# Optimization experiments

Hardware: AMD Instinct MI355X
Metric: run time of the kernel (lower is better)

## Reference

```python
import math
import jax, jax.numpy as jnp
import numpy as np

B, L, D, H = 2, 2048, 1024, 16
HD = D // H
EPS = 1e-6
ROPE_BASE = 10000.0


def setup_inputs() -> dict:
    key = jax.random.key(0)
    ks = jax.random.split(key, 6)
    s = 0.02
    return {
        "z_H_previous": jax.random.normal(ks[0], (B, L, D), jnp.float32),
        "z_L_current": jax.random.normal(ks[1], (B, L, D), jnp.float32),
        "w_qkv": jax.random.normal(ks[2], (3 * D, D), jnp.float32) * s,
        "w_out": jax.random.normal(ks[3], (D, D), jnp.float32) * s,
        "w_ffn1": jax.random.normal(ks[4], (4 * D, D), jnp.float32) * s,
        "w_ffn2": jax.random.normal(ks[5], (D, 4 * D), jnp.float32) * s,
        "g_norm1": jnp.ones((D,), jnp.float32),
        "g_norm2": jnp.ones((D,), jnp.float32),
    }


def _rmsnorm(x, g):
    # mean of squares over last dim, rsqrt, scale
    ms = jnp.mean(x * x, axis=-1, keepdims=True)
    return x * jax.lax.rsqrt(ms + EPS) * g


def _rope(x):
    # x: [b, h, l, hd]; non-interleaved rotate-half RoPE
    l, d = x.shape[-2], x.shape[-1]
    half = d // 2
    inv_freq = 1.0 / (ROPE_BASE ** (jnp.arange(half, dtype=jnp.float32) / half))
    freqs = jnp.arange(l, dtype=jnp.float32)[:, None] * inv_freq[None, :]  # [l, half]
    cos, sin = jnp.cos(freqs), jnp.sin(freqs)
    x1, x2 = x[..., :half], x[..., half:]
    return jnp.concatenate([x1 * cos - x2 * sin, x2 * cos + x1 * sin], axis=-1)


def reference(z_H_previous, z_L_current, w_qkv, w_out, w_ffn1, w_ffn2, g_norm1, g_norm2):
    x = z_H_previous + z_L_current                       # [b, l, d]
    h = _rmsnorm(x, g_norm1)
    b, l, d = h.shape
    qkv = h @ w_qkv.T                                    # [b, l, 3d]
    qkv = qkv.reshape(b, l, 3, H, HD).transpose(2, 0, 3, 1, 4)  # [3, b, h, l, hd]
    q, k, v = qkv[0], qkv[1], qkv[2]
    q = _rope(q)
    k = _rope(k)
    scores = jnp.einsum("bhqd,bhkd->bhqk", q, k) / math.sqrt(HD)
    attn = jax.nn.softmax(scores, axis=-1)
    out = jnp.einsum("bhqk,bhkd->bhqd", attn, v)         # [b, h, l, hd]
    out = out.transpose(0, 2, 1, 3).reshape(b, l, d)
    x = x + out @ w_out.T
    h2 = _rmsnorm(x, g_norm2)
    ffn = jax.nn.silu(h2 @ w_ffn1.T) @ w_ffn2.T
    return x + ffn
```

## Files before the change

### kernel.cpp

```cpp
#include <hip/hip_runtime.h>

typedef __bf16 bf16;
typedef __bf16 bf16x2 __attribute__((ext_vector_type(2)));
typedef __bf16 bf16x8 __attribute__((ext_vector_type(8)));
typedef __bf16 bf16x4 __attribute__((ext_vector_type(4)));
typedef float  f32x4  __attribute__((ext_vector_type(4)));
typedef float  f32x16 __attribute__((ext_vector_type(16)));
typedef unsigned int uint;

static __device__ __forceinline__ void async_copy16(const void* g, void* l) {
  __builtin_amdgcn_global_load_lds((__attribute__((address_space(1))) void*)g,
                                   (__attribute__((address_space(3))) void*)l,
                                   16, 0, 0);
}

static __device__ __forceinline__ uint pkbf2(float a, float b) {
  union { bf16x2 v; uint u; } x;
  x.v[0] = (bf16)a; x.v[1] = (bf16)b;
  return x.u;
}

union U4 { uint u[4]; bf16x8 v; };

__global__ __launch_bounds__(256)
void f2b_all(const float* __restrict__ s0, const float* __restrict__ s1,
             const float* __restrict__ s2, const float* __restrict__ s3,
             bf16* __restrict__ d0, bf16* __restrict__ d1,
             bf16* __restrict__ d2, bf16* __restrict__ d3) {
  int i = blockIdx.x * 256 + threadIdx.x;
  const float* s; bf16* d; int j;
  if (i < 786432)       { s = s0; d = d0; j = i; }
  else if (i < 1048576) { s = s1; d = d1; j = i - 786432; }
  else if (i < 2097152) { s = s2; d = d2; j = i - 1048576; }
  else                  { s = s3; d = d3; j = i - 2097152; }
  float4 v = ((const float4*)s)[j];
  bf16x4 o;
  o[0] = (bf16)v.x; o[1] = (bf16)v.y; o[2] = (bf16)v.z; o[3] = (bf16)v.w;
  ((bf16x4*)d)[j] = o;
}

__global__ __launch_bounds__(256)
void add_rmsnorm_kernel(const float* __restrict__ a, const float* __restrict__ b,
                        const float* __restrict__ g, float* __restrict__ xout,
                        bf16* __restrict__ hout) {
  const int row = blockIdx.x;
  const int tid = threadIdx.x;
  const size_t base = (size_t)row * 1024 + tid * 4;
  float4 x = *(const float4*)(a + base);
  if (b) {
    float4 y = *(const float4*)(b + base);
    x.x += y.x; x.y += y.y; x.z += y.z; x.w += y.w;
  }
  float ss = x.x*x.x + x.y*x.y + x.z*x.z + x.w*x.w;
#pragma unroll
  for (int off = 32; off > 0; off >>= 1) ss += __shfl_xor(ss, off, 64);
  __shared__ float red[4];
  const int wave = tid >> 6, lane = tid & 63;
  if (lane == 0) red[wave] = ss;
  __syncthreads();
  const float total = red[0] + red[1] + red[2] + red[3];
  const float scale = rsqrtf(total * (1.0f / 1024.0f) + 1e-6f);
  if (xout) *(float4*)(xout + base) = x;
  float4 gv = *(const float4*)(g + tid * 4);
  bf16x4 h;
  h[0] = (bf16)(x.x * scale * gv.x);
  h[1] = (bf16)(x.y * scale * gv.y);
  h[2] = (bf16)(x.z * scale * gv.z);
  h[3] = (bf16)(x.w * scale * gv.w);
  *(bf16x4*)(hout + base) = h;
}

enum { EP_QKV = 0, EP_ADD_RESID = 1, EP_SILU = 2 };

template <int MODE>
__global__ __launch_bounds__(256)
void gemm_bt(const bf16* __restrict__ A, const bf16* __restrict__ W,
             const float* __restrict__ resid, float* __restrict__ outF,
             bf16* __restrict__ outB, bf16* __restrict__ outB2,
             int M, int N, int K) {
  __shared__ bf16 As[128 * 64];
  __shared__ bf16 Bs[128 * 64];
  const int tid  = threadIdx.x;
  const int wave = tid >> 6;
  const int lane = tid & 63;
  const int quad = lane >> 4;
  const int l16  = lane & 15;

  const int bm = blockIdx.x & 31;
  const int bn = blockIdx.x >> 5;
  const int m0 = bm << 7, n0 = bn << 7;
  const int wm = (wave >> 1) << 6;
  const int wn = (wave & 1) << 6;

  const int rl = lane >> 3;
  const int cg = (lane & 7) ^ rl;
  const bf16* gA = A + (size_t)(m0 + wave * 32 + rl) * K + cg * 8;
  const bf16* gB = W + (size_t)(n0 + wave * 32 + rl) * K + cg * 8;

  const int s8 = l16 & 7;
  f32x4 acc[4][4] = {};

  for (int k0 = 0; k0 < K; k0 += 64) {
    __syncthreads();
#pragma unroll
    for (int i = 0; i < 4; i++) {
      async_copy16(gA + (size_t)(i * 8) * K, &As[(wave * 32 + i * 8) * 64]);
      async_copy16(gB + (size_t)(i * 8) * K, &Bs[(wave * 32 + i * 8) * 64]);
    }
    gA += 64; gB += 64;
    __syncthreads();
#pragma unroll
    for (int kh = 0; kh < 2; kh++) {
      bf16x8 af[4], bfr[4];
#pragma unroll
      for (int i = 0; i < 4; i++)
        af[i] = *(const bf16x8*)&As[(wm + i * 16 + l16) * 64 + (((kh * 4 + quad) ^ s8) * 8)];
#pragma unroll
      for (int j = 0; j < 4; j++)
        bfr[j] = *(const bf16x8*)&Bs[(wn + j * 16 + l16) * 64 + (((kh * 4 + quad) ^ s8) * 8)];
#pragma unroll
      for (int i = 0; i < 4; i++)
#pragma unroll
        for (int j = 0; j < 4; j++)
          acc[i][j] = __builtin_amdgcn_mfma_f32_16x16x32_bf16(af[i], bfr[j], acc[i][j], 0, 0, 0);
    }
  }

  if constexpr (MODE == EP_QKV) {
    const int which = n0 >> 10;
    if (which == 2) {
#pragma unroll
      for (int i = 0; i < 4; i++) {
        const int mbase = m0 + wm + i * 16 + quad * 4;
#pragma unroll
        for (int j = 0; j < 4; j++) {
          const int n = n0 + wn + j * 16 + l16;
          const int hh = (n >> 6) & 15, hd = n & 63;
#pragma unroll
          for (int r = 0; r < 4; r++) {
            const int m = mbase + r;
            const int bb = m >> 11, l = m & 2047;
            outB2[((size_t)(bb * 16 + hh) * 64 + hd) * 2048 + l] = (bf16)acc[i][j][r];
          }
        }
      }
    } else {
      const float sc = (which == 0) ? 0.1803368801111243f : 1.0f;
#pragma unroll
      for (int jp = 0; jp < 2; jp++) {
        const int hd1 = jp * 16 + l16;
        const float invf = exp2f(-0.4152410118609203f * (float)hd1);
        const int n1 = n0 + wn + jp * 16 + l16;
        const int hh = (n1 >> 6) & 15;
#pragma unroll
        for (int i = 0; i < 4; i++) {
          const int mbase = m0 + wm + i * 16 + quad * 4;
#pragma unroll
          for (int r = 0; r < 4; r++) {
            const int m = mbase + r;
            const int bb = m >> 11, l = m & 2047;
            float sv, cv;
            sincosf((float)l * invf, &sv, &cv);
            const float x1 = acc[i][jp][r], x2 = acc[i][jp + 2][r];
            const size_t base = (((size_t)(which * 2 + bb) * 16 + hh) * 2048 + l) * 64;
            outB[base + hd1]      = (bf16)((x1 * cv - x2 * sv) * sc);
            outB[base + hd1 + 32] = (bf16)((x2 * cv + x1 * sv) * sc);
          }
        }
      }
    }
  } else {
#pragma unroll
    for (int i = 0; i < 4; i++) {
      const int mbase = m0 + wm + i * 16 + quad * 4;
#pragma unroll
      for (int j = 0; j < 4; j++) {
        const int n = n0 + wn + j * 16 + l16;
        f32x4 v = acc[i][j];
#pragma unroll
        for (int r = 0; r < 4; r++) {
          const int m = mbase + r;
          const float val = v[r];
          if constexpr (MODE == EP_ADD_RESID) {
            outF[(size_t)m * N + n] = val + resid[(size_t)m * N + n];
          } else {
            outB[(size_t)m * N + n] = (bf16)(val / (1.0f + __expf(-val)));
          }
        }
      }
    }
  }
}

__global__ __launch_bounds__(256)
void gemm_bt_splitk(const bf16* __restrict__ A, const bf16* __restrict__ W,
                    float* __restrict__ P, int M, int N, int Ktot) {
  __shared__ bf16 As[128 * 64];
  __shared__ bf16 Bs[128 * 64];
  const int tid  = threadIdx.x;
  const int wave = tid >> 6;
  const int lane = tid & 63;
  const int quad = lane >> 4;
  const int l16  = lane & 15;

  const int r6 = blockIdx.x & 63;
  const int bn = blockIdx.x >> 6;
  const int bm = r6 >> 1;
  const int split = r6 & 1;
  const int m0 = bm << 7, n0 = bn << 7;
  const int wm = (wave >> 1) << 6;
  const int wn = (wave & 1) << 6;
  const int Kh = Ktot >> 1;
  const int koff = split * Kh;

  const int rl = lane >> 3;
  const int cg = (lane & 7) ^ rl;
  const bf16* gA = A + (size_t)(m0 + wave * 32 + rl) * Ktot + koff + cg * 8;
  const bf16* gB = W + (size_t)(n0 + wave * 32 + rl) * Ktot + koff + cg * 8;

  const int s8 = l16 & 7;
  f32x4 acc[4][4] = {};

  for (int k0 = 0; k0 < Kh; k0 += 64) {
    __syncthreads();
#pragma unroll
    for (int i = 0; i < 4; i++) {
      async_copy16(gA + (size_t)(i * 8) * Ktot, &As[(wave * 32 + i * 8) * 64]);
      async_copy16(gB + (size_t)(i * 8) * Ktot, &Bs[(wave * 32 + i * 8) * 64]);
    }
    gA += 64; gB += 64;
    __syncthreads();
#pragma unroll
    for (int kh = 0; kh < 2; kh++) {
      bf16x8 af[4], bfr[4];
#pragma unroll
      for (int i = 0; i < 4; i++)
        af[i] = *(const bf16x8*)&As[(wm + i * 16 + l16) * 64 + (((kh * 4 + quad) ^ s8) * 8)];
#pragma unroll
      for (int j = 0; j < 4; j++)
        bfr[j] = *(const bf16x8*)&Bs[(wn + j * 16 + l16) * 64 + (((kh * 4 + quad) ^ s8) * 8)];
#pragma unroll
      for (int i = 0; i < 4; i++)
#pragma unroll
        for (int j = 0; j < 4; j++)
          acc[i][j] = __builtin_amdgcn_mfma_f32_16x16x32_bf16(af[i], bfr[j], acc[i][j], 0, 0, 0);
    }
  }

  float* Pd = P + (size_t)split * M * N;
#pragma unroll
  for (int i = 0; i < 4; i++) {
    const int mbase = m0 + wm + i * 16 + quad * 4;
#pragma unroll
    for (int j = 0; j < 4; j++) {
      const int n = n0 + wn + j * 16 + l16;
#pragma unroll
      for (int r = 0; r < 4; r++)
        Pd[(size_t)(mbase + r) * N + n] = acc[i][j][r];
    }
  }
}

__global__ __launch_bounds__(256)
void splitk_combine(const float* __restrict__ P, const float* __restrict__ resid,
                    float* __restrict__ out, int total4) {
  int i = blockIdx.x * 256 + threadIdx.x;
  if (i < total4) {
    float4 a = ((const float4*)P)[i];
    float4 b = ((const float4*)(P + 4194304))[i];
    float4 r = ((const float4*)resid)[i];
    float4 o;
    o.x = a.x + b.x + r.x; o.y = a.y + b.y + r.y;
    o.z = a.z + b.z + r.z; o.w = a.w + b.w + r.w;
    ((float4*)out)[i] = o;
  }
}

__global__ __launch_bounds__(256)
void gemm64_bt(const bf16* __restrict__ A, const bf16* __restrict__ W,
               const float* __restrict__ resid, float* __restrict__ outF,
               int M, int N, int K) {
  __shared__ bf16 As[64 * 64];
  __shared__ bf16 Bs[128 * 64];
  const int tid = threadIdx.x, wave = tid >> 6, lane = tid & 63;
  const int quad = lane >> 4, l16 = lane & 15;
  const int bm = blockIdx.x & 63;
  const int bn = blockIdx.x >> 6;
  const int m0 = bm << 6, n0 = bn << 7;
  const int wm = (wave >> 1) * 32, wn = (wave & 1) * 64;

  const int rl = lane >> 3;
  const int cg = (lane & 7) ^ rl;
  const bf16* gA = A + (size_t)(m0 + wave * 16 + rl) * K + cg * 8;
  const bf16* gB = W + (size_t)(n0 + wave * 32 + rl) * K + cg * 8;

  const int s8 = l16 & 7;
  f32x4 acc[2][4] = {};
  for (int k0 = 0; k0 < K; k0 += 64) {
    __syncthreads();
#pragma unroll
    for (int i = 0; i < 2; i++)
      async_copy16(gA + (size_t)(i * 8) * K, &As[(wave * 16 + i * 8) * 64]);
#pragma unroll
    for (int i = 0; i < 4; i++)
      async_copy16(gB + (size_t)(i * 8) * K, &Bs[(wave * 32 + i * 8) * 64]);
    gA += 64; gB += 64;
    __syncthreads();
#pragma unroll
    for (int kh = 0; kh < 2; kh++) {
      bf16x8 af[2], bfr[4];
#pragma unroll
      for (int i = 0; i < 2; i++)
        af[i] = *(const bf16x8*)&As[(wm + i * 16 + l16) * 64 + (((kh * 4 + quad) ^ s8) * 8)];
#pragma unroll
      for (int j = 0; j < 4; j++)
        bfr[j] = *(const bf16x8*)&Bs[(wn + j * 16 + l16) * 64 + (((kh * 4 + quad) ^ s8) * 8)];
#pragma unroll
      for (int i = 0; i < 2; i++)
#pragma unroll
        for (int j = 0; j < 4; j++)
          acc[i][j] = __builtin_amdgcn_mfma_f32_16x16x32_bf16(af[i], bfr[j], acc[i][j], 0, 0, 0);
    }
  }
#pragma unroll
  for (int i = 0; i < 2; i++) {
    const int mbase = m0 + wm + i * 16 + quad * 4;
#pragma unroll
    for (int j = 0; j < 4; j++) {
      const int n = n0 + wn + j * 16 + l16;
#pragma unroll
      for (int r = 0; r < 4; r++) {
        const int m = mbase + r;
        outF[(size_t)m * N + n] = acc[i][j][r] + resid[(size_t)m * N + n];
      }
    }
  }
}

__global__ __launch_bounds__(256, 4)
void attn_kernel(const bf16* __restrict__ qk, const bf16* __restrict__ vt,
                 bf16* __restrict__ Opart, float* __restrict__ Lpart) {
  const int qt    = blockIdx.x & 15;
  const int bh    = (blockIdx.x >> 4) & 31;
  const int split = blockIdx.x >> 9;
  const bf16* Qp = qk + (size_t)bh * 131072;
  const bf16* Kp = Qp + 4194304;
  const bf16* Vp = vt + (size_t)bh * 131072;

  const int tid = threadIdx.x, wave = tid >> 6, lane = tid & 63;
  const int hl = lane >> 5, l32 = lane & 31;
  const int qw = qt * 128 + wave * 32;

  __shared__ bf16 lds[8192];
  bf16* Ks = lds;
  bf16* Vs = lds + 4096;

  bf16x8 qf[4];
#pragma unroll
  for (int dk = 0; dk < 4; dk++)
    qf[dk] = *(const bf16x8*)&Qp[(size_t)(qw + l32) * 64 + dk * 16 + hl * 8];

  f32x16 o0 = {}, o1 = {};
  float sum_acc = 0.0f;

  const int rl = lane >> 3;
  const int cg = (lane & 7) ^ rl;

  const int kvbase = split * 512;
  for (int kv0 = kvbase; kv0 < kvbase + 512; kv0 += 64) {
    __syncthreads();
#pragma unroll
    for (int i = 0; i < 2; i++) {
      const int row = wave * 16 + i * 8;
      async_copy16(Kp + (size_t)(kv0 + row + rl) * 64 + cg * 8, &Ks[row * 64]);
      async_copy16(Vp + (size_t)(row + rl) * 2048 + kv0 + cg * 8, &Vs[row * 64]);
    }
    __syncthreads();

    U4 pf[4];
#pragma unroll
    for (int ks = 0; ks < 2; ks++) {
      f32x16 s = {};
#pragma unroll
      for (int dk = 0; dk < 4; dk++) {
        const bf16x8 kf = *(const bf16x8*)
            &Ks[(ks * 32 + l32) * 64 + ((dk * 2 + hl) ^ (l32 & 7)) * 8];
        s = __builtin_amdgcn_mfma_f32_32x32x16_bf16(kf, qf[dk], s, 0, 0, 0);
      }
      uint d[8];
#pragma unroll
      for (int i = 0; i < 8; i++) {
        const float a = exp2f(s[2 * i]);
        const float b = exp2f(s[2 * i + 1]);
        sum_acc += a + b;
        d[i] = pkbf2(a, b);
      }
      uint send0 = hl ? d[0] : d[2];
      uint send1 = hl ? d[1] : d[3];
      uint send2 = hl ? d[4] : d[6];
      uint send3 = hl ? d[5] : d[7];
      const uint r0 = __shfl_xor(send0, 32, 64);
      const uint r1 = __shfl_xor(send1, 32, 64);
      const uint r2 = __shfl_xor(send2, 32, 64);
      const uint r3 = __shfl_xor(send3, 32, 64);
      U4& f0 = pf[ks * 2];
      U4& f1 = pf[ks * 2 + 1];
      f0.u[0] = hl ? r0 : d[0];  f0.u[1] = hl ? r1 : d[1];
      f0.u[2] = hl ? d[2] : r0;  f0.u[3] = hl ? d[3] : r1;
      f1.u[0] = hl ? r2 : d[4];  f1.u[1] = hl ? r3 : d[5];
      f1.u[2] = hl ? d[6] : r2;  f1.u[3] = hl ? d[7] : r3;
    }

#pragma unroll
    for (int c16 = 0; c16 < 4; c16++) {
      const bf16x8 vf0 = *(const bf16x8*)&Vs[l32 * 64 + ((c16 * 2 + hl) ^ (l32 & 7)) * 8];
      const bf16x8 vf1 = *(const bf16x8*)&Vs[(32 + l32) * 64 + ((c16 * 2 + hl) ^ (l32 & 7)) * 8];
      o0 = __builtin_amdgcn_mfma_f32_32x32x16_bf16(vf0, pf[c16].v, o0, 0, 0, 0);
      o1 = __builtin_amdgcn_mfma_f32_32x32x16_bf16(vf1, pf[c16].v, o1, 0, 0, 0);
    }
  }

  const float l_i = sum_acc + __shfl_xor(sum_acc, 32, 64);
  Lpart[(size_t)(split * 32 + bh) * 2048 + qt * 128 + wave * 32 + l32] = l_i;

  uint* L32 = (uint*)lds;
#pragma unroll
  for (int p = 0; p < 2; p++) {
    __syncthreads();
    if ((wave >> 1) == p) {
      const int lrow = (wave & 1) * 32 + l32;
#pragma unroll
      for (int ds = 0; ds < 2; ds++) {
        const f32x16 ov = ds ? o1 : o0;
#pragma unroll
        for (int i = 0; i < 8; i++) {
          const int r = 2 * i;
          const int dd = ds * 32 + (r & 3) + 8 * (r >> 2) + 4 * hl;
          L32[lrow * 36 + (dd >> 1)] = pkbf2(ov[r], ov[r + 1]);
        }
      }
    }
    __syncthreads();
#pragma unroll
    for (int sp = 0; sp < 2; sp++) {
      const int qr = sp * 32 + (tid >> 3), c = tid & 7;
      const uint4 v = *(const uint4*)&L32[qr * 36 + c * 4];
      *(uint4*)&Opart[(((size_t)(split * 32 + bh) * 2048) + qt * 128 + p * 64 + qr) * 64 + c * 8] = v;
    }
  }
}

__global__ __launch_bounds__(256)
void attn_combine(const bf16* __restrict__ Opart, const float* __restrict__ Lpart,
                  bf16* __restrict__ out) {
  const int t = blockIdx.x * 256 + threadIdx.x;
  const int c = t & 7, qq = t >> 3;
  const int bh = qq >> 11, q = qq & 2047;
  const int b = bh >> 4, h = bh & 15;
  float acc[8] = {};
  float lsum = 0.0f;
#pragma unroll
  for (int s = 0; s < 4; s++) {
    const bf16x8 ov = *(const bf16x8*)&Opart[((size_t)(s * 32 + bh) * 2048 + q) * 64 + c * 8];
    lsum += Lpart[(size_t)(s * 32 + bh) * 2048 + q];
#pragma unroll
    for (int i = 0; i < 8; i++) acc[i] += (float)ov[i];
  }
  const float inv = 1.0f / lsum;
  bf16x8 o;
#pragma unroll
  for (int i = 0; i < 8; i++) o[i] = (bf16)(acc[i] * inv);
  *(bf16x8*)&out[((size_t)b * 2048 + q) * 1024 + h * 64 + c * 8] = o;
}

extern "C" void kernel_launch(void* const* d_in, const int* in_sizes, int n_in,
                              void* d_out, int out_size, void* d_ws, size_t ws_size,
                              hipStream_t stream) {
  (void)in_sizes; (void)n_in; (void)out_size; (void)ws_size;
  const float* zH    = (const float*)d_in[0];
  const float* zL    = (const float*)d_in[1];
  const float* w_qkv = (const float*)d_in[2];
  const float* w_out = (const float*)d_in[3];
  const float* w_f1  = (const float*)d_in[4];
  const float* w_f2  = (const float*)d_in[5];
  const float* g1    = (const float*)d_in[6];
  const float* g2    = (const float*)d_in[7];
  float* out = (float*)d_out;

  char* ws = (char*)d_ws;
  size_t off = 0;
  auto alloc = [&](size_t bytes) {
    void* p = ws + off;
    off += (bytes + 255) & ~(size_t)255;
    return p;
  };
  bf16*  bqkv  = (bf16*)alloc(3145728ull * 2);
  bf16*  bwout = (bf16*)alloc(1048576ull * 2);
  bf16*  bf1   = (bf16*)alloc(4194304ull * 2);
  bf16*  bf2   = (bf16*)alloc(4194304ull * 2);
  const size_t off_x = off;
  float* x     = (float*)alloc(4194304ull * 4);
  bf16*  hbuf  = (bf16*)alloc(4194304ull * 2);
  bf16*  qkb   = (bf16*)alloc(8388608ull * 2);
  bf16*  vtb   = (bf16*)alloc(4194304ull * 2);
  bf16*  attnb = (bf16*)alloc(4194304ull * 2);
  const size_t offU = off;
  float* x2    = (float*)alloc(4194304ull * 4);
  bf16*  h2    = (bf16*)alloc(4194304ull * 2);
  bf16*  act   = (bf16*)alloc(16777216ull * 2);
  bf16*  Opart = (bf16*)(ws + offU);
  float* Lpart = (float*)(ws + offU + 16777216ull * 2 + 256);
  float* Ppart = (float*)(ws + off_x);

  f2b_all<<<12288, 256, 0, stream>>>(w_qkv, w_out, w_f1, w_f2, bqkv, bwout, bf1, bf2);

  add_rmsnorm_kernel<<<4096, 256, 0, stream>>>(zH, zL, g1, x, hbuf);

  gemm_bt<EP_QKV><<<768, 256, 0, stream>>>(hbuf, bqkv, nullptr, nullptr, qkb, vtb,
                                           4096, 3072, 1024);
  attn_kernel<<<2048, 256, 0, stream>>>(qkb, vtb, Opart, Lpart);
  attn_combine<<<2048, 256, 0, stream>>>(Opart, Lpart, attnb);

  gemm64_bt<<<512, 256, 0, stream>>>(attnb, bwout, x, x2, 4096, 1024, 1024);
  add_rmsnorm_kernel<<<4096, 256, 0, stream>>>(x2, nullptr, g2, nullptr, h2);
  gemm_bt<EP_SILU><<<1024, 256, 0, stream>>>(h2, bf1, nullptr, nullptr, act, nullptr,
                                             4096, 4096, 1024);
  gemm_bt_splitk<<<512, 256, 0, stream>>>(act, bf2, Ppart, 4096, 1024, 4096);
  splitk_combine<<<4096, 256, 0, stream>>>(Ppart, x2, out, 1048576);
}
```

Baseline: 372.0 us.

## Permute V sequence layout to drop shuffles in attention P fragment build

```diff
diff --git a/kernel.cpp b/kernel.cpp
--- a/kernel.cpp
+++ b/kernel.cpp
@@ -140,7 +140,8 @@
           for (int r = 0; r < 4; r++) {
             const int m = mbase + r;
             const int bb = m >> 11, l = m & 2047;
-            outB2[((size_t)(bb * 16 + hh) * 64 + hd) * 2048 + l] = (bf16)acc[i][j][r];
+            const int lp = (l & ~15) | (l & 3) | ((l & 4) << 1) | ((l & 8) >> 1);
+            outB2[((size_t)(bb * 16 + hh) * 64 + hd) * 2048 + lp] = (bf16)acc[i][j][r];
           }
         }
       }
@@ -340,9 +341,9 @@
 __global__ __launch_bounds__(256, 4)
 void attn_kernel(const bf16* __restrict__ qk, const bf16* __restrict__ vt,
                  bf16* __restrict__ Opart, float* __restrict__ Lpart) {
-  const int qt    = blockIdx.x & 15;
-  const int bh    = (blockIdx.x >> 4) & 31;
-  const int split = blockIdx.x >> 9;
+  const int qt    = blockIdx.x >> 7;
+  const int bh    = (blockIdx.x >> 2) & 31;
+  const int split = blockIdx.x & 3;
   const bf16* Qp = qk + (size_t)bh * 131072;
   const bf16* Kp = Qp + 4194304;
   const bf16* Vp = vt + (size_t)bh * 131072;
@@ -387,28 +388,15 @@
             &Ks[(ks * 32 + l32) * 64 + ((dk * 2 + hl) ^ (l32 & 7)) * 8];
         s = __builtin_amdgcn_mfma_f32_32x32x16_bf16(kf, qf[dk], s, 0, 0, 0);
       }
-      uint d[8];
-#pragma unroll
-      for (int i = 0; i < 8; i++) {
-        const float a = exp2f(s[2 * i]);
-        const float b = exp2f(s[2 * i + 1]);
-        sum_acc += a + b;
-        d[i] = pkbf2(a, b);
-      }
-      uint send0 = hl ? d[0] : d[2];
-      uint send1 = hl ? d[1] : d[3];
-      uint send2 = hl ? d[4] : d[6];
-      uint send3 = hl ? d[5] : d[7];
-      const uint r0 = __shfl_xor(send0, 32, 64);
-      const uint r1 = __shfl_xor(send1, 32, 64);
-      const uint r2 = __shfl_xor(send2, 32, 64);
-      const uint r3 = __shfl_xor(send3, 32, 64);
-      U4& f0 = pf[ks * 2];
-      U4& f1 = pf[ks * 2 + 1];
-      f0.u[0] = hl ? r0 : d[0];  f0.u[1] = hl ? r1 : d[1];
-      f0.u[2] = hl ? d[2] : r0;  f0.u[3] = hl ? d[3] : r1;
-      f1.u[0] = hl ? r2 : d[4];  f1.u[1] = hl ? r3 : d[5];
-      f1.u[2] = hl ? d[6] : r2;  f1.u[3] = hl ? d[7] : r3;
+#pragma unroll
+      for (int c = 0; c < 2; c++)
+#pragma unroll
+        for (int t = 0; t < 4; t++) {
+          const float a = exp2f(s[c * 8 + 2 * t]);
+          const float b = exp2f(s[c * 8 + 2 * t + 1]);
+          sum_acc += a + b;
+          pf[ks * 2 + c].u[t] = pkbf2(a, b);
+        }
     }
 
 #pragma unroll
```

New measurement: 367.8 us. Within noise of the previous version (-1.1%).
